# Kernel optimization log

Hardware: AMD Instinct MI355X
Metric: run time of the kernel (lower is better)

## Reference

```python
import jax, jax.numpy as jnp
import numpy as np
import math

KERNEL_SIZE = 11
SIGMA = 1.0
STABILIZATION = 1e-06


def _gauss_kernel(k, sigma):
    pad = k // 2
    coords = jnp.arange(k, dtype=jnp.float32) - pad
    yy, xx = jnp.meshgrid(coords, coords, indexing='ij')
    g = jnp.exp(-(xx ** 2 + yy ** 2) / (2.0 * sigma ** 2))
    return g / g.sum()


def _depthwise_gauss(x, g):
    # x: [B, C, H, W]; g: [K, K]. Zero 'SAME' padding matches nn.Unfold(padding=K//2).
    C = x.shape[1]
    k = g.shape[0]
    w = jnp.broadcast_to(g[None, None], (C, 1, k, k)).astype(x.dtype)
    return jax.lax.conv_general_dilated(
        x, w, window_strides=(1, 1), padding='SAME',
        feature_group_count=C,
        dimension_numbers=('NCHW', 'OIHW', 'NCHW'))


def setup_inputs() -> dict:
    key = jax.random.key(0)
    x = jax.random.normal(key, (16, 64, 256, 256), dtype=jnp.float32)
    return {"x": x}


def reference(x):
    g = _gauss_kernel(KERNEL_SIZE, SIGMA)
    # Weighted local mean and second moment; since sum(g)=1:
    # var = E_w[x^2] - (E_w[x])^2  ==  sum_w (x - mean)^2  (same math as the torch module)
    mean = _depthwise_gauss(x, g)
    ex2 = _depthwise_gauss(x * x, g)
    var = ex2 - mean * mean + STABILIZATION
    return jnp.sqrt(var)
```

## Files before the change

### kernel.cpp

```cpp
#include <hip/hip_runtime.h>
#include <math.h>


#define W        256
#define IMG_PIX  (W * W)
#define BANDH    32

#define GW0 1.4867195e-06f
#define GW1 1.3383023e-04f
#define GW2 4.4318485e-03f
#define GW3 5.3990965e-02f
#define GW4 2.4197072e-01f
#define GW5 3.9894228e-01f

typedef float f4 __attribute__((ext_vector_type(4)));

__device__ __forceinline__ f4 vfma(float g, f4 a, f4 c) {
    f4 gv = {g, g, g, g};
    return __builtin_elementwise_fma(gv, a, c);
}

__device__ __forceinline__ f4 load_row(const float* __restrict__ xi, int gr, int c) {
    if ((unsigned)gr < (unsigned)W)
        return *(const f4*)(xi + (size_t)gr * W + c);
    return (f4){0.f, 0.f, 0.f, 0.f};
}

__device__ __forceinline__ f4 shfl_up1(f4 v) {
    f4 r;
    r.x = __shfl_up(v.x, 1);
    r.y = __shfl_up(v.y, 1);
    r.z = __shfl_up(v.z, 1);
    r.w = __shfl_up(v.w, 1);
    return r;
}
__device__ __forceinline__ f4 shfl_dn1(f4 v) {
    f4 r;
    r.x = __shfl_down(v.x, 1);
    r.y = __shfl_down(v.y, 1);
    r.z = __shfl_down(v.z, 1);
    r.w = __shfl_down(v.w, 1);
    return r;
}

__device__ __forceinline__ void hpass(f4 v, float mu1, float mu2,
                                      float md1, float md2, float h[4]) {
    f4 L = shfl_up1(v);
    float eL = __shfl_up(v.w, 2) * mu2;
    f4 R = shfl_dn1(v);
    float eR = __shfl_down(v.x, 2) * md2;
    L *= mu1;
    R *= md1;
    float F[14] = { eL,  L.x, L.y, L.z, L.w,
                    v.x, v.y, v.z, v.w,
                    R.x, R.y, R.z, R.w,  eR };
    #pragma unroll
    for (int j = 0; j < 4; ++j) {
        float s = GW5 * F[j + 5];
        s = fmaf(GW4, F[j + 4] + F[j + 6],  s);
        s = fmaf(GW3, F[j + 3] + F[j + 7],  s);
        s = fmaf(GW2, F[j + 2] + F[j + 8],  s);
        s = fmaf(GW1, F[j + 1] + F[j + 9],  s);
        s = fmaf(GW0, F[j + 0] + F[j + 10], s);
        h[j] = s;
    }
}

template<int K>
__device__ __forceinline__ void row_step(const float* __restrict__ xi,
                                         float* __restrict__ oi,
                                         f4 (&xw)[11], f4& pf,
                                         int c, int grow,
                                         float mu1, float mu2,
                                         float md1, float md2) {
    constexpr int SN = (K + 10) % 11;
    xw[SN] = pf;
    f4 pn = load_row(xi, grow + 6, c);

    constexpr int SC = (K + 5) % 11;
    f4 xc = xw[SC];
    f4 v1 = xc * GW5;
    f4 v2 = (xc * xc) * GW5;
    #define VPAIR(D, G) { constexpr int A_ = (K + 5 - (D)) % 11;                 \
                          constexpr int B_ = (K + 5 + (D)) % 11;                 \
                          f4 xa_ = xw[A_], xb_ = xw[B_];                         \
                          v1 = vfma(G, xa_ + xb_, v1);                           \
                          f4 sq_ = __builtin_elementwise_fma(xb_, xb_, xa_*xa_); \
                          v2 = vfma(G, sq_, v2); }
    VPAIR(1, GW4) VPAIR(2, GW3) VPAIR(3, GW2) VPAIR(4, GW1) VPAIR(5, GW0)
    #undef VPAIR

    float h1[4], h2[4];
    hpass(v1, mu1, mu2, md1, md2, h1);
    hpass(v2, mu1, mu2, md1, md2, h2);

    f4 o;
    o.x = sqrtf(fmaf(-h1[0], h1[0], h2[0]) + 1e-6f);
    o.y = sqrtf(fmaf(-h1[1], h1[1], h2[1]) + 1e-6f);
    o.z = sqrtf(fmaf(-h1[2], h1[2], h2[2]) + 1e-6f);
    o.w = sqrtf(fmaf(-h1[3], h1[3], h2[3]) + 1e-6f);
    *(f4*)(oi + (size_t)grow * W + c) = o;

    pf = pn;
}

__global__ __launch_bounds__(256, 4) void
local_std_kernel(const float* __restrict__ x, float* __restrict__ out) {
    const int t    = threadIdx.x;
    const int wv   = t >> 6;
    const int lane = t & 63;
    const int bid  = blockIdx.x;
    const int img  = bid >> 1;
    const int half = bid & 1;
    const float* xi = x   + (size_t)img * IMG_PIX;
    float*       oi = out + (size_t)img * IMG_PIX;

    const int c  = lane << 2;
    const int r0 = half * (W / 2) + wv * BANDH;

    const float mu1 = (lane >= 1)  ? 1.f : 0.f;
    const float mu2 = (lane >= 2)  ? 1.f : 0.f;
    const float md1 = (lane <= 62) ? 1.f : 0.f;
    const float md2 = (lane <= 61) ? 1.f : 0.f;

    f4 xw[11];
    #pragma unroll
    for (int i = 0; i < 10; ++i)
        xw[i] = load_row(xi, r0 - 5 + i, c);
    xw[10] = (f4){0.f, 0.f, 0.f, 0.f};
    f4 pf = load_row(xi, r0 + 5, c);

    #pragma unroll 1
    for (int ii = 0; ii < 3; ++ii) {
        const int base = ii * 11;
        #define STEP(k) if (base + (k) < BANDH) \
            row_step<(k)>(xi, oi, xw, pf, c, r0 + base + (k), mu1, mu2, md1, md2);
        STEP(0) STEP(1) STEP(2) STEP(3) STEP(4) STEP(5)
        STEP(6) STEP(7) STEP(8) STEP(9) STEP(10)
        #undef STEP
    }
}

extern "C" void kernel_launch(void* const* d_in, const int* in_sizes, int n_in,
                              void* d_out, int out_size, void* d_ws, size_t ws_size,
                              hipStream_t stream) {
    const float* x  = (const float*)d_in[0];
    float* out      = (float*)d_out;
    const int n_img = in_sizes[0] / IMG_PIX;
    local_std_kernel<<<dim3(n_img * 2), 256, 0, stream>>>(x, out);
}
```

Measured before the change: 451.6 us.

## Swap separable pass order: horizontal filter per input row, then vertical over cached rows

Applies the horizontal Gaussian pass (with cross-lane shuffles) once per incoming row and keeps a ring buffer of horizontally filtered mean and squared rows. The vertical pass then runs over these buffered results. Shuffles and horizontal FMAs are done once per input row, with squaring done before the shuffle-derived taps. The cost is two 11-entry f4 register ring buffers instead of one, which raises register pressure and may reduce occupancy under launch_bounds(256,4).

```diff
diff --git a/kernel.cpp b/kernel.cpp
--- a/kernel.cpp
+++ b/kernel.cpp
@@ -43,8 +43,9 @@
     return r;
 }
 
-__device__ __forceinline__ void hpass(f4 v, float mu1, float mu2,
-                                      float md1, float md2, float h[4]) {
+__device__ __forceinline__ void hrow(f4 v, float mu1, float mu2,
+                                     float md1, float md2,
+                                     f4& h1, f4& h2) {
     f4 L = shfl_up1(v);
     float eL = __shfl_up(v.w, 2) * mu2;
     f4 R = shfl_dn1(v);
@@ -54,6 +55,7 @@
     float F[14] = { eL,  L.x, L.y, L.z, L.w,
                     v.x, v.y, v.z, v.w,
                     R.x, R.y, R.z, R.w,  eR };
+    float o1[4], o2[4];
     #pragma unroll
     for (int j = 0; j < 4; ++j) {
         float s = GW5 * F[j + 5];
@@ -62,43 +64,52 @@
         s = fmaf(GW2, F[j + 2] + F[j + 8],  s);
         s = fmaf(GW1, F[j + 1] + F[j + 9],  s);
         s = fmaf(GW0, F[j + 0] + F[j + 10], s);
-        h[j] = s;
+        o1[j] = s;
     }
+    #pragma unroll
+    for (int k = 0; k < 14; ++k)
+        F[k] = F[k] * F[k];
+    #pragma unroll
+    for (int j = 0; j < 4; ++j) {
+        float s = GW5 * F[j + 5];
+        s = fmaf(GW4, F[j + 4] + F[j + 6],  s);
+        s = fmaf(GW3, F[j + 3] + F[j + 7],  s);
+        s = fmaf(GW2, F[j + 2] + F[j + 8],  s);
+        s = fmaf(GW1, F[j + 1] + F[j + 9],  s);
+        s = fmaf(GW0, F[j + 0] + F[j + 10], s);
+        o2[j] = s;
+    }
+    h1 = (f4){o1[0], o1[1], o1[2], o1[3]};
+    h2 = (f4){o2[0], o2[1], o2[2], o2[3]};
 }
 
 template<int K>
 __device__ __forceinline__ void row_step(const float* __restrict__ xi,
                                          float* __restrict__ oi,
-                                         f4 (&xw)[11], f4& pf,
+                                         f4 (&r1)[11], f4 (&r2)[11], f4& pf,
                                          int c, int grow,
                                          float mu1, float mu2,
                                          float md1, float md2) {
-    constexpr int SN = (K + 10) % 11;
-    xw[SN] = pf;
     f4 pn = load_row(xi, grow + 6, c);
 
+    constexpr int SN = (K + 10) % 11;
+    hrow(pf, mu1, mu2, md1, md2, r1[SN], r2[SN]);
+
     constexpr int SC = (K + 5) % 11;
-    f4 xc = xw[SC];
-    f4 v1 = xc * GW5;
-    f4 v2 = (xc * xc) * GW5;
-    #define VPAIR(D, G) { constexpr int A_ = (K + 5 - (D)) % 11;                 \
-                          constexpr int B_ = (K + 5 + (D)) % 11;                 \
-                          f4 xa_ = xw[A_], xb_ = xw[B_];                         \
-                          v1 = vfma(G, xa_ + xb_, v1);                           \
-                          f4 sq_ = __builtin_elementwise_fma(xb_, xb_, xa_*xa_); \
-                          v2 = vfma(G, sq_, v2); }
+    f4 v1 = r1[SC] * GW5;
+    f4 v2 = r2[SC] * GW5;
+    #define VPAIR(D, G) { constexpr int A_ = (K + 5 - (D)) % 11;    \
+                          constexpr int B_ = (K + 5 + (D)) % 11;    \
+                          v1 = vfma(G, r1[A_] + r1[B_], v1);        \
+                          v2 = vfma(G, r2[A_] + r2[B_], v2); }
     VPAIR(1, GW4) VPAIR(2, GW3) VPAIR(3, GW2) VPAIR(4, GW1) VPAIR(5, GW0)
     #undef VPAIR
 
-    float h1[4], h2[4];
-    hpass(v1, mu1, mu2, md1, md2, h1);
-    hpass(v2, mu1, mu2, md1, md2, h2);
-
     f4 o;
-    o.x = sqrtf(fmaf(-h1[0], h1[0], h2[0]) + 1e-6f);
-    o.y = sqrtf(fmaf(-h1[1], h1[1], h2[1]) + 1e-6f);
-    o.z = sqrtf(fmaf(-h1[2], h1[2], h2[2]) + 1e-6f);
-    o.w = sqrtf(fmaf(-h1[3], h1[3], h2[3]) + 1e-6f);
+    o.x = sqrtf(fmaf(-v1.x, v1.x, v2.x) + 1e-6f);
+    o.y = sqrtf(fmaf(-v1.y, v1.y, v2.y) + 1e-6f);
+    o.z = sqrtf(fmaf(-v1.z, v1.z, v2.z) + 1e-6f);
+    o.w = sqrtf(fmaf(-v1.w, v1.w, v2.w) + 1e-6f);
     *(f4*)(oi + (size_t)grow * W + c) = o;
 
     pf = pn;
@@ -123,18 +134,21 @@
     const float md1 = (lane <= 62) ? 1.f : 0.f;
     const float md2 = (lane <= 61) ? 1.f : 0.f;
 
-    f4 xw[11];
+    f4 r1[11], r2[11];
     #pragma unroll
-    for (int i = 0; i < 10; ++i)
-        xw[i] = load_row(xi, r0 - 5 + i, c);
-    xw[10] = (f4){0.f, 0.f, 0.f, 0.f};
+    for (int i = 0; i < 10; ++i) {
+        f4 xr = load_row(xi, r0 - 5 + i, c);
+        hrow(xr, mu1, mu2, md1, md2, r1[i], r2[i]);
+    }
+    r1[10] = (f4){0.f, 0.f, 0.f, 0.f};
+    r2[10] = (f4){0.f, 0.f, 0.f, 0.f};
     f4 pf = load_row(xi, r0 + 5, c);
 
     #pragma unroll 1
     for (int ii = 0; ii < 3; ++ii) {
         const int base = ii * 11;
         #define STEP(k) if (base + (k) < BANDH) \
-            row_step<(k)>(xi, oi, xw, pf, c, r0 + base + (k), mu1, mu2, md1, md2);
+            row_step<(k)>(xi, oi, r1, r2, pf, c, r0 + base + (k), mu1, mu2, md1, md2);
         STEP(0) STEP(1) STEP(2) STEP(3) STEP(4) STEP(5)
         STEP(6) STEP(7) STEP(8) STEP(9) STEP(10)
         #undef STEP
```

After: 831.2 us. +84.0%, slower.
